# Performance work log

Measured on AMD Instinct MI355X. Metric: run time of the kernel, lower is better.

## Reference

```python
import jax, jax.numpy as jnp
import numpy as np

# Solver constants (from init_kwargs)
LB = 0.0        # lower bound of bisection interval
UB = 100.0      # upper bound
STEP = 1e-4     # convergence tolerance
K = 30.0        # sigmoid sharpness for soft bisection update


def dual_derivative(x, m):
    """Concrete dual derivative: x [bs, s], m [bs] -> [bs].
    Monotone increasing in m; root near per-sample median of x."""
    return jnp.mean(jax.nn.sigmoid(K * (m[:, None] - x)), axis=1) - 0.5


def setup_inputs() -> dict:
    key = jax.random.key(0)
    bs, s = 4096, 2048
    x = jax.random.uniform(key, (bs, s), jnp.float32) * (UB - LB) + LB
    return {"x": x}


def reference(x):
    bs = x.shape[0]
    # interval halves exactly each iteration: (ub'-lb') = (ub-lb)/2
    n_iters = int(np.ceil(np.log2((UB - LB) / (2.0 * STEP))))  # = 19

    lb = jnp.full((bs,), LB, dtype=x.dtype)
    ub = jnp.full((bs,), UB, dtype=x.dtype)
    m = jnp.zeros((bs,), dtype=x.dtype)
    # active == (not found) and (ub - lb > 2*step), checked at loop top
    active = jnp.ones((bs,), dtype=bool)

    def body(carry, _):
        lb, ub, m, active = carry
        m_new = jnp.where(active, (lb + ub) * 0.5, m)
        Dm = dual_derivative(x, m_new)                  # [bs]
        found = jnp.abs(Dm) < STEP
        H = jax.nn.sigmoid(K * Dm)
        lb_new = jnp.where(active, m_new - H * (m_new - lb), lb)
        ub_new = jnp.where(active, ub - H * (ub - m_new), ub)
        active_new = active & (~found) & (ub_new - lb_new > 2.0 * STEP)
        return (lb_new, ub_new, m_new, active_new), None

    (lb, ub, m, active), _ = jax.lax.scan(body, (lb, ub, m, active), None, length=n_iters)
    return m.reshape(-1, 1)
```

## Files before the change

### kernel.cpp

```cpp
#include <hip/hip_runtime.h>


constexpr int   S_DIM = 2048;
constexpr int   EPL   = S_DIM / 64;
constexpr float KL2E  = 43.280851308343876f;
constexpr int   BANDC = 128;
constexpr float BHW   = 1.7f;
constexpr float MCL   = 1.1f;
constexpr int   NNEWT = 4;

template<int CTRL, int RMASK>
__device__ __forceinline__ int dpp_add_i(int v) {
    return v + __builtin_amdgcn_update_dpp(0, v, CTRL, RMASK, 0xF, true);
}

__device__ __forceinline__ int wave_iscan_incl(int v) {
    v = dpp_add_i<0x111, 0xF>(v);
    v = dpp_add_i<0x112, 0xF>(v);
    v = dpp_add_i<0x114, 0xF>(v);
    v = dpp_add_i<0x118, 0xF>(v);
    v = dpp_add_i<0x142, 0xA>(v);
    v = dpp_add_i<0x143, 0xC>(v);
    return v;
}

template<int CTRL>
__device__ __forceinline__ float dpp_add_f(float v) {
    int sh = __builtin_amdgcn_update_dpp(0, __float_as_int(v), CTRL, 0xF, 0xF, true);
    return v + __int_as_float(sh);
}

__device__ __forceinline__ float wave_reduce_bcast(float v) {
    v = dpp_add_f<0x111>(v);
    v = dpp_add_f<0x112>(v);
    v = dpp_add_f<0x114>(v);
    v = dpp_add_f<0x118>(v);
    v = dpp_add_f<0x142>(v);
    v = dpp_add_f<0x143>(v);
    return __int_as_float(__builtin_amdgcn_readlane(__float_as_int(v), 63));
}

__device__ __forceinline__ float sig(float xv, float m) {
    float e = __builtin_amdgcn_exp2f((xv - m) * KL2E);
    return __builtin_amdgcn_rcpf(1.0f + e);
}

__global__ __launch_bounds__(256)
void dicho_kernel(const float* __restrict__ x, float* __restrict__ out, int bs) {
    __shared__ float band[4][BANDC];

    const int wave = threadIdx.x >> 6;
    const int lane = threadIdx.x & 63;
    const int row  = blockIdx.x * 4 + wave;
    if (row >= bs) return;

    const float4* xr = reinterpret_cast<const float4*>(x + (size_t)row * S_DIM);
    float xs[EPL];
    #pragma unroll
    for (int j = 0; j < EPL / 4; ++j) {
        float4 v = xr[j * 64 + lane];
        xs[4*j+0] = v.x; xs[4*j+1] = v.y; xs[4*j+2] = v.z; xs[4*j+3] = v.w;
    }

    int n50 = 0;
    #pragma unroll
    for (int j = 0; j < EPL; ++j)
        n50 += __popcll(__ballot(xs[j] < 50.0f));
    float c0 = 50.0f + (float)(S_DIM / 2 - n50) * (100.0f / (float)S_DIM);
    c0 = fminf(100.0f, fmaxf(0.0f, c0));

    const float blo = c0 - BHW, bhi = c0 + BHW;
    int below_l = 0, nb_l = 0;
    #pragma unroll
    for (int j = 0; j < EPL; ++j) {
        below_l += (xs[j] < blo) ? 1 : 0;
        nb_l    += (xs[j] >= blo && xs[j] <= bhi) ? 1 : 0;
    }
    const int packed = (below_l << 16) | nb_l;
    const int pincl  = wave_iscan_incl(packed);
    const int ptot   = __builtin_amdgcn_readlane(pincl, 63);
    const int belowN = ptot >> 16;
    const int nbtot  = ptot & 0xffff;

    float m;
    const bool ok = (nbtot <= BANDC) && (belowN < S_DIM / 2)
                 && (belowN + nbtot > S_DIM / 2);
    if (ok) {
        int k = (pincl - packed) & 0xffff;
        #pragma unroll
        for (int j = 0; j < EPL; ++j) {
            if (xs[j] >= blo && xs[j] <= bhi) band[wave][k++] = xs[j];
        }
        const bool v0 = lane < nbtot, v1 = lane + 64 < nbtot;
        const float a0 = band[wave][lane];
        const float a1 = band[wave][lane + 64];
        const float below = (float)belowN;

        float Lb = c0 - MCL, Rb = c0 + MCL;
        m = c0;
        #pragma unroll
        for (int t = 0; t < NNEWT; ++t) {
            const float r0 = sig(a0, m), r1 = sig(a1, m);
            const float S = (v0 ? r0 : 0.0f) + (v1 ? r1 : 0.0f);
            const float T = (v0 ? r0 * (1.0f - r0) : 0.0f)
                          + (v1 ? r1 * (1.0f - r1) : 0.0f);
            const float Stot = wave_reduce_bcast(S) + below;
            const float Ttot = wave_reduce_bcast(T);
            const float D  = Stot * (1.0f / (float)S_DIM) - 0.5f;
            const float Dp = Ttot * (30.0f / (float)S_DIM);
            if (D > 0.0f) Rb = m; else Lb = m;
            float mn = m - D * __builtin_amdgcn_rcpf(Dp + 1e-20f);
            if (!(mn > Lb && mn < Rb)) mn = (Lb + Rb) * 0.5f;
            m = mn;
        }
    } else {
        float lo = 0.0f, hi = 100.0f;
        #pragma unroll 1
        for (int t = 0; t < 16; ++t) {
            const float c = (lo + hi) * 0.5f;
            int cnt = 0;
            #pragma unroll
            for (int j = 0; j < EPL; ++j)
                cnt += __popcll(__ballot(xs[j] < c));
            if (cnt >= S_DIM / 2) hi = c; else lo = c;
        }
        m = (lo + hi) * 0.5f;
        #pragma unroll 1
        for (int t = 0; t < 3; ++t) {
            float S = 0.0f, T = 0.0f;
            #pragma unroll
            for (int j = 0; j < EPL; ++j) {
                const float r = sig(xs[j], m);
                S += r;
                T += r * (1.0f - r);
            }
            S = wave_reduce_bcast(S);
            T = wave_reduce_bcast(T);
            const float D  = S * (1.0f / (float)S_DIM) - 0.5f;
            const float Dp = T * (30.0f / (float)S_DIM);
            float step = D * __builtin_amdgcn_rcpf(Dp + 1e-12f);
            step = fminf(0.5f, fmaxf(-0.5f, step));
            m -= step;
        }
    }

    if (lane == 0) out[row] = m;
}

extern "C" void kernel_launch(void* const* d_in, const int* in_sizes, int n_in,
                              void* d_out, int out_size, void* d_ws, size_t ws_size,
                              hipStream_t stream) {
    const float* x = (const float*)d_in[0];
    float* out = (float*)d_out;
    const int bs = out_size;
    const int blocks = (bs + 3) / 4;
    dicho_kernel<<<blocks, 256, 0, stream>>>(x, out, bs);
}
```

Baseline: 10.97 us.

## Split each row across two waves with LDS cross-wave reductions

Each row is now handled by two 64-lane waves instead of one, so each lane holds 16 elements instead of 32, and twice as many blocks are launched. Per-wave counts and partial sums are combined through small shared-memory arrays guarded by __syncthreads. The band is gathered from both waves, and only one wave runs the Newton refinement. The aim is to raise occupancy and memory-level parallelism on a bandwidth- and latency-bound kernel. The cost is block-wide barriers, and the fast path is now taken only when both rows in a block qualify for it.

```diff
diff --git a/kernel.cpp b/kernel.cpp
--- a/kernel.cpp
+++ b/kernel.cpp
@@ -2,7 +2,7 @@
 
 
 constexpr int   S_DIM = 2048;
-constexpr int   EPL   = S_DIM / 64;
+constexpr int   EPL   = S_DIM / 128;
 constexpr float KL2E  = 43.280851308343876f;
 constexpr int   BANDC = 128;
 constexpr float BHW   = 1.7f;
@@ -22,6 +22,10 @@
     v = dpp_add_i<0x142, 0xA>(v);
     v = dpp_add_i<0x143, 0xC>(v);
     return v;
+}
+
+__device__ __forceinline__ int wave_isum(int v) {
+    return __builtin_amdgcn_readlane(wave_iscan_incl(v), 63);
 }
 
 template<int CTRL>
@@ -45,27 +49,37 @@
     return __builtin_amdgcn_rcpf(1.0f + e);
 }
 
-__global__ __launch_bounds__(256)
+__global__ __launch_bounds__(256, 8)
 void dicho_kernel(const float* __restrict__ x, float* __restrict__ out, int bs) {
-    __shared__ float band[4][BANDC];
+    __shared__ int   icomm[2][2];
+    __shared__ int   pcomm[2][2];
+    __shared__ float scomm[2][2][2];
+    __shared__ float band[2][BANDC];
 
-    const int wave = threadIdx.x >> 6;
+    const int wid  = threadIdx.x >> 6;
     const int lane = threadIdx.x & 63;
-    const int row  = blockIdx.x * 4 + wave;
-    if (row >= bs) return;
+    const int pair = wid >> 1;
+    const int wv   = wid & 1;
+    int row = blockIdx.x * 2 + pair;
+    const bool valid = (row < bs);
+    if (!valid) row = bs - 1;
 
     const float4* xr = reinterpret_cast<const float4*>(x + (size_t)row * S_DIM);
+    const int li = wv * 64 + lane;
     float xs[EPL];
     #pragma unroll
     for (int j = 0; j < EPL / 4; ++j) {
-        float4 v = xr[j * 64 + lane];
+        float4 v = xr[j * 128 + li];
         xs[4*j+0] = v.x; xs[4*j+1] = v.y; xs[4*j+2] = v.z; xs[4*j+3] = v.w;
     }
 
-    int n50 = 0;
+    int c50 = 0;
     #pragma unroll
-    for (int j = 0; j < EPL; ++j)
-        n50 += __popcll(__ballot(xs[j] < 50.0f));
+    for (int j = 0; j < EPL; ++j) c50 += (xs[j] < 50.0f) ? 1 : 0;
+    const int w50 = wave_isum(c50);
+    if (lane == 0) icomm[pair][wv] = w50;
+    __syncthreads();
+    const int n50 = icomm[pair][0] + icomm[pair][1];
     float c0 = 50.0f + (float)(S_DIM / 2 - n50) * (100.0f / (float)S_DIM);
     c0 = fminf(100.0f, fmaxf(0.0f, c0));
 
@@ -78,53 +92,72 @@
     }
     const int packed = (below_l << 16) | nb_l;
     const int pincl  = wave_iscan_incl(packed);
-    const int ptot   = __builtin_amdgcn_readlane(pincl, 63);
-    const int belowN = ptot >> 16;
-    const int nbtot  = ptot & 0xffff;
+    const int wtot   = __builtin_amdgcn_readlane(pincl, 63);
+    if (lane == 0) pcomm[pair][wv] = wtot;
+    __syncthreads();
+    const int t00 = pcomm[0][0], t01 = pcomm[0][1];
+    const int t10 = pcomm[1][0], t11 = pcomm[1][1];
+    const int ta = pair ? t10 : t00, tb = pair ? t11 : t01;
+    const int belowN = (ta >> 16) + (tb >> 16);
+    const int nb0    = ta & 0xffff;
+    const int nbtot  = nb0 + (tb & 0xffff);
 
-    float m;
-    const bool ok = (nbtot <= BANDC) && (belowN < S_DIM / 2)
-                 && (belowN + nbtot > S_DIM / 2);
-    if (ok) {
-        int k = (pincl - packed) & 0xffff;
+    const int  b0  = (t00 >> 16) + (t01 >> 16);
+    const int  n0  = (t00 & 0xffff) + (t01 & 0xffff);
+    const int  b1  = (t10 >> 16) + (t11 >> 16);
+    const int  n1  = (t10 & 0xffff) + (t11 & 0xffff);
+    const bool ok0 = (n0 <= BANDC) && (b0 < S_DIM/2) && (b0 + n0 > S_DIM/2);
+    const bool ok1 = (n1 <= BANDC) && (b1 < S_DIM/2) && (b1 + n1 > S_DIM/2);
+    const bool allok = ok0 && ok1;
+
+    if (allok) {
+        int k = ((pincl - packed) & 0xffff) + (wv ? nb0 : 0);
         #pragma unroll
         for (int j = 0; j < EPL; ++j) {
-            if (xs[j] >= blo && xs[j] <= bhi) band[wave][k++] = xs[j];
+            if (xs[j] >= blo && xs[j] <= bhi) band[pair][k++] = xs[j];
         }
-        const bool v0 = lane < nbtot, v1 = lane + 64 < nbtot;
-        const float a0 = band[wave][lane];
-        const float a1 = band[wave][lane + 64];
-        const float below = (float)belowN;
+        __syncthreads();
 
-        float Lb = c0 - MCL, Rb = c0 + MCL;
-        m = c0;
-        #pragma unroll
-        for (int t = 0; t < NNEWT; ++t) {
-            const float r0 = sig(a0, m), r1 = sig(a1, m);
-            const float S = (v0 ? r0 : 0.0f) + (v1 ? r1 : 0.0f);
-            const float T = (v0 ? r0 * (1.0f - r0) : 0.0f)
-                          + (v1 ? r1 * (1.0f - r1) : 0.0f);
-            const float Stot = wave_reduce_bcast(S) + below;
-            const float Ttot = wave_reduce_bcast(T);
-            const float D  = Stot * (1.0f / (float)S_DIM) - 0.5f;
-            const float Dp = Ttot * (30.0f / (float)S_DIM);
-            if (D > 0.0f) Rb = m; else Lb = m;
-            float mn = m - D * __builtin_amdgcn_rcpf(Dp + 1e-20f);
-            if (!(mn > Lb && mn < Rb)) mn = (Lb + Rb) * 0.5f;
-            m = mn;
+        if (wv == 0) {
+            const bool  v0 = lane < nbtot, v1 = lane + 64 < nbtot;
+            const float a0 = band[pair][lane];
+            const float a1 = band[pair][lane + 64];
+            const float below = (float)belowN;
+
+            float Lb = c0 - MCL, Rb = c0 + MCL, m = c0;
+            #pragma unroll
+            for (int t = 0; t < NNEWT; ++t) {
+                const float r0 = sig(a0, m), r1 = sig(a1, m);
+                const float S = (v0 ? r0 : 0.0f) + (v1 ? r1 : 0.0f);
+                const float T = (v0 ? r0 * (1.0f - r0) : 0.0f)
+                              + (v1 ? r1 * (1.0f - r1) : 0.0f);
+                const float Stot = wave_reduce_bcast(S) + below;
+                const float Ttot = wave_reduce_bcast(T);
+                const float D  = Stot * (1.0f / (float)S_DIM) - 0.5f;
+                const float Dp = Ttot * (30.0f / (float)S_DIM);
+                if (D > 0.0f) Rb = m; else Lb = m;
+                float mn = m - D * __builtin_amdgcn_rcpf(Dp + 1e-20f);
+                if (!(mn > Lb && mn < Rb)) mn = (Lb + Rb) * 0.5f;
+                m = mn;
+            }
+            if (valid && lane == 0) out[row] = m;
         }
     } else {
         float lo = 0.0f, hi = 100.0f;
         #pragma unroll 1
         for (int t = 0; t < 16; ++t) {
             const float c = (lo + hi) * 0.5f;
-            int cnt = 0;
+            int cl = 0;
             #pragma unroll
-            for (int j = 0; j < EPL; ++j)
-                cnt += __popcll(__ballot(xs[j] < c));
+            for (int j = 0; j < EPL; ++j) cl += (xs[j] < c) ? 1 : 0;
+            const int wc = wave_isum(cl);
+            if (lane == 0) icomm[pair][wv] = wc;
+            __syncthreads();
+            const int cnt = icomm[pair][0] + icomm[pair][1];
+            __syncthreads();
             if (cnt >= S_DIM / 2) hi = c; else lo = c;
         }
-        m = (lo + hi) * 0.5f;
+        float m = (lo + hi) * 0.5f;
         #pragma unroll 1
         for (int t = 0; t < 3; ++t) {
             float S = 0.0f, T = 0.0f;
@@ -136,15 +169,19 @@
             }
             S = wave_reduce_bcast(S);
             T = wave_reduce_bcast(T);
-            const float D  = S * (1.0f / (float)S_DIM) - 0.5f;
-            const float Dp = T * (30.0f / (float)S_DIM);
+            if (lane == 0) { scomm[pair][wv][0] = S; scomm[pair][wv][1] = T; }
+            __syncthreads();
+            const float St = scomm[pair][0][0] + scomm[pair][1][0];
+            const float Tt = scomm[pair][0][1] + scomm[pair][1][1];
+            __syncthreads();
+            const float D  = St * (1.0f / (float)S_DIM) - 0.5f;
+            const float Dp = Tt * (30.0f / (float)S_DIM);
             float step = D * __builtin_amdgcn_rcpf(Dp + 1e-12f);
             step = fminf(0.5f, fmaxf(-0.5f, step));
             m -= step;
         }
+        if (valid && wv == 0 && lane == 0) out[row] = m;
     }
-
-    if (lane == 0) out[row] = m;
 }
 
 extern "C" void kernel_launch(void* const* d_in, const int* in_sizes, int n_in,
@@ -153,6 +190,6 @@
     const float* x = (const float*)d_in[0];
     float* out = (float*)d_out;
     const int bs = out_size;
-    const int blocks = (bs + 3) / 4;
+    const int blocks = (bs + 1) / 2;
     dicho_kernel<<<blocks, 256, 0, stream>>>(x, out, bs);
 }
```

New measurement: 11.34 us. +3.3%, slower.

## Process two rows per wave with both loads issued upfront; count via DPP scan

Applied to the files above, without the earlier changes.

Each wave now handles two rows. It loads both rows' data into registers before solving either, so the second row's memory latency is hidden behind the first row's compute. The count below 50 is now a per-lane comparison sum plus a DPP scan, replacing 32 ballot/popcount pairs. The cost is more VGPRs, which may lower occupancy, half as many blocks in the grid, and the shared band buffer being reused for both rows in sequence.

```diff
diff --git a/kernel.cpp b/kernel.cpp
--- a/kernel.cpp
+++ b/kernel.cpp
@@ -8,6 +8,7 @@
 constexpr float BHW   = 1.7f;
 constexpr float MCL   = 1.1f;
 constexpr int   NNEWT = 4;
+constexpr int   RPW   = 2;
 
 template<int CTRL, int RMASK>
 __device__ __forceinline__ int dpp_add_i(int v) {
@@ -45,27 +46,21 @@
     return __builtin_amdgcn_rcpf(1.0f + e);
 }
 
-__global__ __launch_bounds__(256)
-void dicho_kernel(const float* __restrict__ x, float* __restrict__ out, int bs) {
-    __shared__ float band[4][BANDC];
-
-    const int wave = threadIdx.x >> 6;
-    const int lane = threadIdx.x & 63;
-    const int row  = blockIdx.x * 4 + wave;
-    if (row >= bs) return;
-
-    const float4* xr = reinterpret_cast<const float4*>(x + (size_t)row * S_DIM);
+__device__ __forceinline__ float solve_row(const float4 (&v4)[EPL / 4],
+                                           float* bandp, int lane) {
     float xs[EPL];
+    int c50 = 0;
     #pragma unroll
     for (int j = 0; j < EPL / 4; ++j) {
-        float4 v = xr[j * 64 + lane];
-        xs[4*j+0] = v.x; xs[4*j+1] = v.y; xs[4*j+2] = v.z; xs[4*j+3] = v.w;
+        xs[4*j+0] = v4[j].x; xs[4*j+1] = v4[j].y;
+        xs[4*j+2] = v4[j].z; xs[4*j+3] = v4[j].w;
+        c50 += (v4[j].x < 50.0f) ? 1 : 0;
+        c50 += (v4[j].y < 50.0f) ? 1 : 0;
+        c50 += (v4[j].z < 50.0f) ? 1 : 0;
+        c50 += (v4[j].w < 50.0f) ? 1 : 0;
     }
 
-    int n50 = 0;
-    #pragma unroll
-    for (int j = 0; j < EPL; ++j)
-        n50 += __popcll(__ballot(xs[j] < 50.0f));
+    const int n50 = __builtin_amdgcn_readlane(wave_iscan_incl(c50), 63);
     float c0 = 50.0f + (float)(S_DIM / 2 - n50) * (100.0f / (float)S_DIM);
     c0 = fminf(100.0f, fmaxf(0.0f, c0));
 
@@ -82,22 +77,20 @@
     const int belowN = ptot >> 16;
     const int nbtot  = ptot & 0xffff;
 
-    float m;
     const bool ok = (nbtot <= BANDC) && (belowN < S_DIM / 2)
                  && (belowN + nbtot > S_DIM / 2);
     if (ok) {
         int k = (pincl - packed) & 0xffff;
         #pragma unroll
         for (int j = 0; j < EPL; ++j) {
-            if (xs[j] >= blo && xs[j] <= bhi) band[wave][k++] = xs[j];
+            if (xs[j] >= blo && xs[j] <= bhi) bandp[k++] = xs[j];
         }
-        const bool v0 = lane < nbtot, v1 = lane + 64 < nbtot;
-        const float a0 = band[wave][lane];
-        const float a1 = band[wave][lane + 64];
+        const bool  v0 = lane < nbtot, v1 = lane + 64 < nbtot;
+        const float a0 = bandp[lane];
+        const float a1 = bandp[lane + 64];
         const float below = (float)belowN;
 
-        float Lb = c0 - MCL, Rb = c0 + MCL;
-        m = c0;
+        float Lb = c0 - MCL, Rb = c0 + MCL, m = c0;
         #pragma unroll
         for (int t = 0; t < NNEWT; ++t) {
             const float r0 = sig(a0, m), r1 = sig(a1, m);
@@ -113,38 +106,67 @@
             if (!(mn > Lb && mn < Rb)) mn = (Lb + Rb) * 0.5f;
             m = mn;
         }
-    } else {
-        float lo = 0.0f, hi = 100.0f;
-        #pragma unroll 1
-        for (int t = 0; t < 16; ++t) {
-            const float c = (lo + hi) * 0.5f;
-            int cnt = 0;
-            #pragma unroll
-            for (int j = 0; j < EPL; ++j)
-                cnt += __popcll(__ballot(xs[j] < c));
-            if (cnt >= S_DIM / 2) hi = c; else lo = c;
-        }
-        m = (lo + hi) * 0.5f;
-        #pragma unroll 1
-        for (int t = 0; t < 3; ++t) {
-            float S = 0.0f, T = 0.0f;
-            #pragma unroll
-            for (int j = 0; j < EPL; ++j) {
-                const float r = sig(xs[j], m);
-                S += r;
-                T += r * (1.0f - r);
-            }
-            S = wave_reduce_bcast(S);
-            T = wave_reduce_bcast(T);
-            const float D  = S * (1.0f / (float)S_DIM) - 0.5f;
-            const float Dp = T * (30.0f / (float)S_DIM);
-            float step = D * __builtin_amdgcn_rcpf(Dp + 1e-12f);
-            step = fminf(0.5f, fmaxf(-0.5f, step));
-            m -= step;
-        }
+        return m;
     }
 
-    if (lane == 0) out[row] = m;
+    float lo = 0.0f, hi = 100.0f;
+    #pragma unroll 1
+    for (int t = 0; t < 16; ++t) {
+        const float c = (lo + hi) * 0.5f;
+        int cnt = 0;
+        #pragma unroll
+        for (int j = 0; j < EPL; ++j)
+            cnt += __popcll(__ballot(xs[j] < c));
+        if (cnt >= S_DIM / 2) hi = c; else lo = c;
+    }
+    float m = (lo + hi) * 0.5f;
+    #pragma unroll 1
+    for (int t = 0; t < 3; ++t) {
+        float S = 0.0f, T = 0.0f;
+        #pragma unroll
+        for (int j = 0; j < EPL; ++j) {
+            const float r = sig(xs[j], m);
+            S += r;
+            T += r * (1.0f - r);
+        }
+        S = wave_reduce_bcast(S);
+        T = wave_reduce_bcast(T);
+        const float D  = S * (1.0f / (float)S_DIM) - 0.5f;
+        const float Dp = T * (30.0f / (float)S_DIM);
+        float step = D * __builtin_amdgcn_rcpf(Dp + 1e-12f);
+        step = fminf(0.5f, fmaxf(-0.5f, step));
+        m -= step;
+    }
+    return m;
+}
+
+__global__ __launch_bounds__(256)
+void dicho_kernel(const float* __restrict__ x, float* __restrict__ out, int bs) {
+    __shared__ float band[4][BANDC];
+
+    const int wid  = threadIdx.x >> 6;
+    const int lane = threadIdx.x & 63;
+    const int g    = blockIdx.x * 4 + wid;
+    const int rowA = g * RPW;
+    const int rowB = rowA + 1;
+    if (rowA >= bs) return;
+    const bool hasB = (rowB < bs);
+
+    const float4* xrA = reinterpret_cast<const float4*>(x + (size_t)rowA * S_DIM);
+    const float4* xrB = reinterpret_cast<const float4*>(x + (size_t)(hasB ? rowB : rowA) * S_DIM);
+    float4 va[EPL / 4], vb[EPL / 4];
+    #pragma unroll
+    for (int j = 0; j < EPL / 4; ++j) va[j] = xrA[j * 64 + lane];
+    #pragma unroll
+    for (int j = 0; j < EPL / 4; ++j) vb[j] = xrB[j * 64 + lane];
+
+    const float mA = solve_row(va, band[wid], lane);
+    if (lane == 0) out[rowA] = mA;
+
+    if (hasB) {
+        const float mB = solve_row(vb, band[wid], lane);
+        if (lane == 0) out[rowB] = mB;
+    }
 }
 
 extern "C" void kernel_launch(void* const* d_in, const int* in_sizes, int n_in,
@@ -153,6 +175,7 @@
     const float* x = (const float*)d_in[0];
     float* out = (float*)d_out;
     const int bs = out_size;
-    const int blocks = (bs + 3) / 4;
+    const int waves  = (bs + RPW - 1) / RPW;
+    const int blocks = (waves + 3) / 4;
     dicho_kernel<<<blocks, 256, 0, stream>>>(x, out, bs);
 }
```

Measured after the change: 12.33 us. 12.4% more time.

## Compact fixed median band during load and validate bracket before Newton

Applied to the files above, without the earlier changes.

Elements in a fixed window [42,58) are compacted into shared memory as they are loaded, using a per-chunk wave scan, so the full 32-element register array is no longer kept live on the fast path. The band is larger (up to 448 entries, 7 per lane), and two extra sigmoid evaluations check that the root is bracketed before the Newton iterations run. When the check fails, the row is reloaded from global memory and goes through the bisection fallback. This trades lower register pressure and a single load pass against more sigmoid work per iteration and a scan per load chunk.

```diff
diff --git a/kernel.cpp b/kernel.cpp
--- a/kernel.cpp
+++ b/kernel.cpp
@@ -4,9 +4,9 @@
 constexpr int   S_DIM = 2048;
 constexpr int   EPL   = S_DIM / 64;
 constexpr float KL2E  = 43.280851308343876f;
-constexpr int   BANDC = 128;
-constexpr float BHW   = 1.7f;
-constexpr float MCL   = 1.1f;
+constexpr float SLO   = 42.0f, SHI = 58.0f;
+constexpr int   CAP   = 448;
+constexpr float BRH   = 1.1f;
 constexpr int   NNEWT = 4;
 
 template<int CTRL, int RMASK>
@@ -47,73 +47,105 @@
 
 __global__ __launch_bounds__(256)
 void dicho_kernel(const float* __restrict__ x, float* __restrict__ out, int bs) {
-    __shared__ float band[4][BANDC];
+    __shared__ float band[4][CAP];
 
-    const int wave = threadIdx.x >> 6;
+    const int wid  = threadIdx.x >> 6;
     const int lane = threadIdx.x & 63;
-    const int row  = blockIdx.x * 4 + wave;
+    const int row  = blockIdx.x * 4 + wid;
     if (row >= bs) return;
+    float* bandp = band[wid];
 
     const float4* xr = reinterpret_cast<const float4*>(x + (size_t)row * S_DIM);
-    float xs[EPL];
+
+    int cpk = 0;
+    int k   = 0;
     #pragma unroll
     for (int j = 0; j < EPL / 4; ++j) {
-        float4 v = xr[j * 64 + lane];
-        xs[4*j+0] = v.x; xs[4*j+1] = v.y; xs[4*j+2] = v.z; xs[4*j+3] = v.w;
+        const float4 v = xr[j * 64 + lane];
+        const bool m0 = (v.x >= SLO) && (v.x < SHI);
+        const bool m1 = (v.y >= SLO) && (v.y < SHI);
+        const bool m2 = (v.z >= SLO) && (v.z < SHI);
+        const bool m3 = (v.w >= SLO) && (v.w < SHI);
+        cpk += ((v.x < SLO) ? 0x10000 : 0) + ((v.x < 50.0f) ? 1 : 0)
+             + ((v.y < SLO) ? 0x10000 : 0) + ((v.y < 50.0f) ? 1 : 0)
+             + ((v.z < SLO) ? 0x10000 : 0) + ((v.z < 50.0f) ? 1 : 0)
+             + ((v.w < SLO) ? 0x10000 : 0) + ((v.w < 50.0f) ? 1 : 0);
+        const int mb   = (int)m0 + (int)m1 + (int)m2 + (int)m3;
+        const int incl = wave_iscan_incl(mb);
+        int base = k + incl - mb;
+        if (m0) { if (base < CAP) bandp[base] = v.x; base++; }
+        if (m1) { if (base < CAP) bandp[base] = v.y; base++; }
+        if (m2) { if (base < CAP) bandp[base] = v.z; base++; }
+        if (m3) { if (base < CAP) bandp[base] = v.w; base++; }
+        k += __builtin_amdgcn_readlane(incl, 63);
     }
 
-    int n50 = 0;
-    #pragma unroll
-    for (int j = 0; j < EPL; ++j)
-        n50 += __popcll(__ballot(xs[j] < 50.0f));
-    float c0 = 50.0f + (float)(S_DIM / 2 - n50) * (100.0f / (float)S_DIM);
-    c0 = fminf(100.0f, fmaxf(0.0f, c0));
+    const int ptot = __builtin_amdgcn_readlane(wave_iscan_incl(cpk), 63);
+    const int n42  = ptot >> 16;
+    const int n50  = ptot & 0xffff;
+    const float c0 = 50.0f + (float)(S_DIM / 2 - n50) * (100.0f / (float)S_DIM);
 
-    const float blo = c0 - BHW, bhi = c0 + BHW;
-    int below_l = 0, nb_l = 0;
-    #pragma unroll
-    for (int j = 0; j < EPL; ++j) {
-        below_l += (xs[j] < blo) ? 1 : 0;
-        nb_l    += (xs[j] >= blo && xs[j] <= bhi) ? 1 : 0;
+    float m = 0.0f;
+    bool done = false;
+
+    if (k <= CAP && c0 >= 44.9f && c0 <= 55.1f) {
+        const bool  w0 = lane < k,       w1 = lane + 64  < k;
+        const bool  w2 = lane + 128 < k, w3 = lane + 192 < k;
+        const bool  w4 = lane + 256 < k, w5 = lane + 320 < k;
+        const bool  w6 = lane + 384 < k;
+        const float a0 = bandp[lane],       a1 = bandp[lane + 64];
+        const float a2 = bandp[lane + 128], a3 = bandp[lane + 192];
+        const float a4 = bandp[lane + 256], a5 = bandp[lane + 320];
+        const float a6 = bandp[lane + 384];
+        const float below = (float)n42;
+
+        auto evalD = [&](float mm, float& D, float& Dp, bool needDp) {
+            const float r0 = sig(a0, mm), r1 = sig(a1, mm), r2 = sig(a2, mm);
+            const float r3 = sig(a3, mm), r4 = sig(a4, mm), r5 = sig(a5, mm);
+            const float r6 = sig(a6, mm);
+            float S = (w0 ? r0 : 0.0f) + (w1 ? r1 : 0.0f) + (w2 ? r2 : 0.0f)
+                    + (w3 ? r3 : 0.0f) + (w4 ? r4 : 0.0f) + (w5 ? r5 : 0.0f)
+                    + (w6 ? r6 : 0.0f);
+            D = (wave_reduce_bcast(S) + below) * (1.0f / (float)S_DIM) - 0.5f;
+            if (needDp) {
+                float T = (w0 ? r0 * (1.0f - r0) : 0.0f)
+                        + (w1 ? r1 * (1.0f - r1) : 0.0f)
+                        + (w2 ? r2 * (1.0f - r2) : 0.0f)
+                        + (w3 ? r3 * (1.0f - r3) : 0.0f)
+                        + (w4 ? r4 * (1.0f - r4) : 0.0f)
+                        + (w5 ? r5 * (1.0f - r5) : 0.0f)
+                        + (w6 ? r6 * (1.0f - r6) : 0.0f);
+                Dp = wave_reduce_bcast(T) * (30.0f / (float)S_DIM);
+            }
+        };
+
+        float Lb = c0 - BRH, Rb = c0 + BRH;
+        float DL, DR, dum;
+        evalD(Lb, DL, dum, false);
+        evalD(Rb, DR, dum, false);
+
+        if (DL < 0.0f && DR > 0.0f) {
+            m = c0;
+            #pragma unroll
+            for (int t = 0; t < NNEWT; ++t) {
+                float D, Dp;
+                evalD(m, D, Dp, true);
+                if (D > 0.0f) Rb = m; else Lb = m;
+                float mn = m - D * __builtin_amdgcn_rcpf(Dp + 1e-20f);
+                if (!(mn > Lb && mn < Rb)) mn = (Lb + Rb) * 0.5f;
+                m = mn;
+            }
+            done = true;
+        }
     }
-    const int packed = (below_l << 16) | nb_l;
-    const int pincl  = wave_iscan_incl(packed);
-    const int ptot   = __builtin_amdgcn_readlane(pincl, 63);
-    const int belowN = ptot >> 16;
-    const int nbtot  = ptot & 0xffff;
 
-    float m;
-    const bool ok = (nbtot <= BANDC) && (belowN < S_DIM / 2)
-                 && (belowN + nbtot > S_DIM / 2);
-    if (ok) {
-        int k = (pincl - packed) & 0xffff;
+    if (!done) {
+        float xs[EPL];
         #pragma unroll
-        for (int j = 0; j < EPL; ++j) {
-            if (xs[j] >= blo && xs[j] <= bhi) band[wave][k++] = xs[j];
+        for (int j = 0; j < EPL / 4; ++j) {
+            float4 v = xr[j * 64 + lane];
+            xs[4*j+0] = v.x; xs[4*j+1] = v.y; xs[4*j+2] = v.z; xs[4*j+3] = v.w;
         }
-        const bool v0 = lane < nbtot, v1 = lane + 64 < nbtot;
-        const float a0 = band[wave][lane];
-        const float a1 = band[wave][lane + 64];
-        const float below = (float)belowN;
-
-        float Lb = c0 - MCL, Rb = c0 + MCL;
-        m = c0;
-        #pragma unroll
-        for (int t = 0; t < NNEWT; ++t) {
-            const float r0 = sig(a0, m), r1 = sig(a1, m);
-            const float S = (v0 ? r0 : 0.0f) + (v1 ? r1 : 0.0f);
-            const float T = (v0 ? r0 * (1.0f - r0) : 0.0f)
-                          + (v1 ? r1 * (1.0f - r1) : 0.0f);
-            const float Stot = wave_reduce_bcast(S) + below;
-            const float Ttot = wave_reduce_bcast(T);
-            const float D  = Stot * (1.0f / (float)S_DIM) - 0.5f;
-            const float Dp = Ttot * (30.0f / (float)S_DIM);
-            if (D > 0.0f) Rb = m; else Lb = m;
-            float mn = m - D * __builtin_amdgcn_rcpf(Dp + 1e-20f);
-            if (!(mn > Lb && mn < Rb)) mn = (Lb + Rb) * 0.5f;
-            m = mn;
-        }
-    } else {
         float lo = 0.0f, hi = 100.0f;
         #pragma unroll 1
         for (int t = 0; t < 16; ++t) {
```

Result: slower. 18.98 us (+73.0%).
